# Performance work log

Hardware: AMD Instinct MI355X
Metric: run time of the kernel (lower is better)

Reference implementation:

```python
import jax, jax.numpy as jnp
import numpy as np

LN_EPS = 1e-5

def _layernorm(x, gamma, beta):
    # x: [B, 4, H]; gamma/beta: [4, H]; computed in fp32 as the torch subclass does
    x32 = x.astype(jnp.float32)
    mu = jnp.mean(x32, axis=-1, keepdims=True)
    var = jnp.mean(jnp.square(x32 - mu), axis=-1, keepdims=True)
    y = (x32 - mu) * jax.lax.rsqrt(var + LN_EPS)
    return (y * gamma + beta).astype(x.dtype)

def setup_inputs() -> dict:
    key = jax.random.key(0)
    ks = jax.random.split(key, 6)
    B, I, H = 8192, 512, 1024
    x = jax.random.normal(ks[0], (B, I), dtype=jnp.float32)
    h = jax.random.normal(ks[1], (B, H), dtype=jnp.float32)
    c = jax.random.normal(ks[2], (B, H), dtype=jnp.float32)
    Wi = jax.random.normal(ks[3], (I, 4 * H), dtype=jnp.float32) * (1.0 / np.sqrt(I))
    Wh = jax.random.normal(ks[4], (H, 4 * H), dtype=jnp.float32) * (1.0 / np.sqrt(H))
    bh = jax.random.normal(ks[5], (4 * H,), dtype=jnp.float32) * 0.01
    ln_gamma = jnp.ones((4, H), dtype=jnp.float32)
    ln_beta = jnp.zeros((4, H), dtype=jnp.float32)
    return {"x": x, "h": h, "c": c, "Wi": Wi, "Wh": Wh, "bh": bh,
            "ln_gamma": ln_gamma, "ln_beta": ln_beta}

def reference(x, h, c, Wi, Wh, bh, ln_gamma, ln_beta):
    B = x.shape[0]
    H = h.shape[-1]
    gates = x @ Wi + h @ Wh + bh            # [B, 4H]
    gates = gates.reshape(B, 4, H)           # chunk into i, f, g, o
    gates = _layernorm(gates, ln_gamma, ln_beta)
    i, f, g, o = gates[:, 0], gates[:, 1], gates[:, 2], gates[:, 3]
    c_new = jax.nn.sigmoid(f) * c + jax.nn.sigmoid(i) * jnp.tanh(g)
    h_new = jax.nn.sigmoid(o) * jnp.tanh(c_new)   # layer_norm_c is Identity
    return (h_new, c_new)
```

## Files before the change

kernel.cpp:

```cpp
#include <hip/hip_runtime.h>
#include <stdint.h>

#define BATCH 8192
#define IDIM  512
#define HDIM  1024
#define KDIM  1536
#define NDIM  4096

typedef __bf16 bf16x8 __attribute__((ext_vector_type(8)));
typedef float  f32x4  __attribute__((ext_vector_type(4)));
typedef unsigned short u16x8 __attribute__((ext_vector_type(8)));

__device__ __forceinline__ unsigned short f2bf(float f) {
    union { float f; unsigned u; } v; v.f = f;
    unsigned r = v.u + 0x7fffu + ((v.u >> 16) & 1u);
    return (unsigned short)(r >> 16);
}
__device__ __forceinline__ float bf2f(unsigned short u) {
    union { unsigned u; float f; } v; v.u = ((unsigned)u) << 16;
    return v.f;
}
__device__ __forceinline__ float fexp(float x) {
    return __builtin_amdgcn_exp2f(x * 1.44269504f);
}
__device__ __forceinline__ float sigm(float x) {
    return __builtin_amdgcn_rcpf(1.f + fexp(-x));
}
__device__ __forceinline__ float ftanh(float x) {
    return 1.f - 2.f * __builtin_amdgcn_rcpf(1.f + fexp(2.f * x));
}

__device__ __forceinline__ void load16(void* lds, const void* g) {
    __builtin_amdgcn_global_load_lds(
        (const __attribute__((address_space(1))) unsigned int*)g,
        (__attribute__((address_space(3))) unsigned int*)lds, 16, 0, 0);
}

#define NPACKA (BATCH * KDIM / 4 / 256)
#define NPACKW ((NDIM / 32) * (KDIM / 32))
__global__ __launch_bounds__(256) void pack_ab(const float* __restrict__ x,
                                               const float* __restrict__ h,
                                               const float* __restrict__ Wi,
                                               const float* __restrict__ Wh,
                                               unsigned short* __restrict__ A,
                                               unsigned short* __restrict__ Wt) {
    __shared__ float tile[32][33];
    int blk = blockIdx.x;
    if (blk < NPACKA) {
        int idx = blk * 256 + threadIdx.x;
        int row = idx / (KDIM / 4);
        int g   = idx % (KDIM / 4);
        int col = g * 4;
        float4 v;
        if (col < IDIM) v = ((const float4*)(x + (size_t)row * IDIM))[g];
        else            v = ((const float4*)(h + (size_t)row * HDIM))[(col - IDIM) / 4];
        ushort4 o;
        o.x = f2bf(v.x); o.y = f2bf(v.y); o.z = f2bf(v.z); o.w = f2bf(v.w);
        ((ushort4*)A)[idx] = o;
    } else {
        int b  = blk - NPACKA;
        int n0 = (b & 127) * 32;
        int k0 = (b >> 7) * 32;
        int tx = threadIdx.x & 31, ty = threadIdx.x >> 5;
#pragma unroll
        for (int j = 0; j < 4; j++) {
            int k = k0 + ty + 8 * j;
            float v;
            if (k < IDIM) v = Wi[(size_t)k * NDIM + n0 + tx];
            else          v = Wh[(size_t)(k - IDIM) * NDIM + n0 + tx];
            tile[ty + 8 * j][tx] = v;
        }
        __syncthreads();
#pragma unroll
        for (int j = 0; j < 4; j++)
            Wt[(size_t)(n0 + ty + 8 * j) * KDIM + k0 + tx] = f2bf(tile[tx][ty + 8 * j]);
    }
}

__global__ __launch_bounds__(512, 2) void gemm_bt(const unsigned short* __restrict__ A,
                                                  const unsigned short* __restrict__ Bt,
                                                  unsigned short* __restrict__ C) {
    __shared__ __align__(16) unsigned short smem[65536];

    const int t    = threadIdx.x;
    const int wave = t >> 6;
    const int lane = t & 63;
    const int lrow = lane & 15;
    const int quad = lane >> 4;

    const int bid = blockIdx.x;
    const int xcd = bid & 7;
    const int jj  = bid >> 3;
    const int bm  = (xcd * 4 + (jj & 3)) * 256;
    const int bn  = (jj >> 2) * 256;

    const int wm = (wave & 1) * 128;
    const int wn = (wave >> 1) * 64;

    int srcA[2], srcB[2];
#pragma unroll
    for (int j = 0; j < 2; j++) {
        int q   = t + 512 * j;
        int rp  = q >> 3, s = q & 7;
        int xx  = s ^ (rp & 7);
        int row = 2 * rp + (xx >> 2);
        int kc  = xx & 3;
        srcA[j] = (bm + row) * KDIM + kc * 8;
        srcB[j] = (bn + row) * KDIM + kc * 8;
    }

    int offA[8], offB[4];
#pragma unroll
    for (int mt = 0; mt < 8; mt++) {
        int r = wm + mt * 16 + lrow;
        offA[mt] = (r >> 1) * 64 + (((((r & 1) << 2) | quad) ^ ((r >> 1) & 7)) * 8);
    }
#pragma unroll
    for (int nt = 0; nt < 4; nt++) {
        int r = wn + nt * 16 + lrow;
        offB[nt] = (r >> 1) * 64 + (((((r & 1) << 2) | quad) ^ ((r >> 1) & 7)) * 8);
    }

    f32x4 acc[8][4] = {};

#define STAGE(tt) do {                                              \
    unsigned short* _d = smem + (((tt) & 3) << 14);                 \
    const int _ko = (tt) * 32;                                      \
    load16(_d +          t * 8, A  + (size_t)(srcA[0] + _ko));      \
    load16(_d +  4096 +  t * 8, A  + (size_t)(srcA[1] + _ko));      \
    load16(_d +  8192 +  t * 8, Bt + (size_t)(srcB[0] + _ko));      \
    load16(_d + 12288 +  t * 8, Bt + (size_t)(srcB[1] + _ko));      \
} while (0)

    STAGE(0); STAGE(1); STAGE(2);

    const int NT = KDIM / 32;
    for (int T = 0; T < NT; ++T) {
        if (T < NT - 2)       asm volatile("s_waitcnt vmcnt(8)" ::: "memory");
        else if (T == NT - 2) asm volatile("s_waitcnt vmcnt(4)" ::: "memory");
        else                  asm volatile("s_waitcnt vmcnt(0)" ::: "memory");
        __builtin_amdgcn_s_barrier();
        __builtin_amdgcn_sched_barrier(0);

        const unsigned short* bufA = smem + ((T & 3) << 14);
        const unsigned short* bufB = bufA + 8192;

        bf16x8 a[8], b[4];
        a[0] = *(const bf16x8*)(bufA + offA[0]);
        b[0] = *(const bf16x8*)(bufB + offB[0]);
        b[1] = *(const bf16x8*)(bufB + offB[1]);
        b[2] = *(const bf16x8*)(bufB + offB[2]);
        b[3] = *(const bf16x8*)(bufB + offB[3]);
        if (T + 3 < NT) STAGE(T + 3);

#pragma unroll
        for (int mt = 0; mt < 8; mt++) {
            if (mt < 7) a[mt + 1] = *(const bf16x8*)(bufA + offA[mt + 1]);
#pragma unroll
            for (int nt = 0; nt < 4; nt++)
                acc[mt][nt] = __builtin_amdgcn_mfma_f32_16x16x32_bf16(
                    a[mt], b[nt], acc[mt][nt], 0, 0, 0);
        }
    }
#undef STAGE

#pragma unroll
    for (int mt = 0; mt < 8; mt++)
#pragma unroll
        for (int nt = 0; nt < 4; nt++) {
            int row = bm + wm + mt * 16 + quad * 4;
            int col = bn + wn + nt * 16 + lrow;
#pragma unroll
            for (int r = 0; r < 4; r++)
                C[(size_t)(row + r) * NDIM + col] = f2bf(acc[mt][nt][r]);
        }
}

__global__ __launch_bounds__(256) void lstm_ep(const unsigned short* __restrict__ gates,
                                               const float* __restrict__ bh,
                                               const float* __restrict__ c,
                                               const float* __restrict__ gamma,
                                               const float* __restrict__ beta,
                                               float* __restrict__ out) {
    const int wave = threadIdx.x >> 6;
    const int lane = threadIdx.x & 63;
    const int b    = blockIdx.x * 4 + wave;
    const int col0 = lane * 16;

    const unsigned short* gr = gates + (size_t)b * NDIM;
    float v[4][16];
    float s[4], sq[4];
#pragma unroll
    for (int g = 0; g < 4; g++) {
        const unsigned short* gp = gr + g * HDIM + col0;
        u16x8 ga = *(const u16x8*)gp;
        u16x8 gb = *(const u16x8*)(gp + 8);
        float bb[16];
#pragma unroll
        for (int q = 0; q < 4; q++)
            *(float4*)(bb + 4 * q) = ((const float4*)(bh + g * HDIM + col0))[q];
        float ls = 0.f, lq = 0.f;
#pragma unroll
        for (int j = 0; j < 16; j++) {
            float tv = bf2f(j < 8 ? ga[j] : gb[j - 8]) + bb[j];
            v[g][j] = tv; ls += tv; lq += tv * tv;
        }
        s[g] = ls; sq[g] = lq;
    }
#pragma unroll
    for (int off = 32; off; off >>= 1) {
#pragma unroll
        for (int g = 0; g < 4; g++) {
            s[g]  += __shfl_xor(s[g], off);
            sq[g] += __shfl_xor(sq[g], off);
        }
    }
#pragma unroll
    for (int g = 0; g < 4; g++) {
        const float mu  = s[g] * (1.f / HDIM);
        const float var = sq[g] * (1.f / HDIM) - mu * mu;
        const float rs  = rsqrtf(var + 1e-5f);
        float gm[16], bt[16];
#pragma unroll
        for (int q = 0; q < 4; q++) {
            *(float4*)(gm + 4 * q) = ((const float4*)(gamma + g * HDIM + col0))[q];
            *(float4*)(bt + 4 * q) = ((const float4*)(beta  + g * HDIM + col0))[q];
        }
#pragma unroll
        for (int j = 0; j < 16; j++) {
            float y = (v[g][j] - mu) * rs * gm[j] + bt[j];
            v[g][j] = (g == 2) ? ftanh(y) : sigm(y);
        }
    }
    const size_t base = (size_t)b * HDIM + col0;
#pragma unroll
    for (int q = 0; q < 4; q++) {
        float4 ci = *(const float4*)(c + base + 4 * q);
        float4 cn, hn;
#pragma unroll
        for (int e = 0; e < 4; e++) {
            int j = 4 * q + e;
            float cnv = v[1][j] * ((float*)&ci)[e] + v[0][j] * v[2][j];
            ((float*)&cn)[e] = cnv;
            ((float*)&hn)[e] = v[3][j] * ftanh(cnv);
        }
        *(float4*)(out + base + 4 * q) = hn;
        *(float4*)(out + (size_t)BATCH * HDIM + base + 4 * q) = cn;
    }
}

extern "C" void kernel_launch(void* const* d_in, const int* in_sizes, int n_in,
                              void* d_out, int out_size, void* d_ws, size_t ws_size,
                              hipStream_t stream) {
    const float* x     = (const float*)d_in[0];
    const float* h     = (const float*)d_in[1];
    const float* c     = (const float*)d_in[2];
    const float* Wi    = (const float*)d_in[3];
    const float* Wh    = (const float*)d_in[4];
    const float* bh    = (const float*)d_in[5];
    const float* gamma = (const float*)d_in[6];
    const float* beta  = (const float*)d_in[7];
    float* out = (float*)d_out;

    unsigned short* A  = (unsigned short*)d_ws;
    unsigned short* Wt = (unsigned short*)((char*)d_ws + (size_t)BATCH * KDIM * 2);
    unsigned short* gates = (unsigned short*)((char*)d_ws + (size_t)BATCH * KDIM * 2
                                                          + (size_t)NDIM * KDIM * 2);

    pack_ab<<<NPACKA + NPACKW, 256, 0, stream>>>(x, h, Wi, Wh, A, Wt);
    gemm_bt<<<dim3((BATCH / 256) * (NDIM / 256)), 512, 0, stream>>>(A, Wt, gates);
    lstm_ep<<<BATCH / 4, 256, 0, stream>>>(gates, bh, c, gamma, beta, out);
}
```

Measured before the change: 298.3 us.

## Pack operands into MFMA fragment layout and load directly from global memory

Packs A and the transposed weights into a fragment-contiguous layout so each MFMA operand fragment is one coalesced 16-byte-per-lane load. The GEMM drops the LDS staging, barriers and swizzle and instead double-buffers fragments in registers straight from global memory. This removes LDS traffic and synchronisation but loses intra-block operand sharing, so waves re-read the same tiles from L2, and latency hiding relies on a single prefetch stage.

```diff
diff --git a/kernel.cpp b/kernel.cpp
--- a/kernel.cpp
+++ b/kernel.cpp
@@ -6,6 +6,7 @@
 #define HDIM  1024
 #define KDIM  1536
 #define NDIM  4096
+#define NKT   (KDIM / 32)
 
 typedef __bf16 bf16x8 __attribute__((ext_vector_type(8)));
 typedef float  f32x4  __attribute__((ext_vector_type(4)));
@@ -30,10 +31,9 @@
     return 1.f - 2.f * __builtin_amdgcn_rcpf(1.f + fexp(2.f * x));
 }
 
-__device__ __forceinline__ void load16(void* lds, const void* g) {
-    __builtin_amdgcn_global_load_lds(
-        (const __attribute__((address_space(1))) unsigned int*)g,
-        (__attribute__((address_space(3))) unsigned int*)lds, 16, 0, 0);
+__device__ __forceinline__ size_t frag_addr(int row, int k) {
+    return ((size_t)((row >> 4) * NKT + (k >> 5)) << 9)
+         + (((row & 15) + 16 * ((k >> 3) & 3)) << 3) + (k & 7);
 }
 
 #define NPACKA (BATCH * KDIM / 4 / 256)
@@ -56,7 +56,7 @@
         else            v = ((const float4*)(h + (size_t)row * HDIM))[(col - IDIM) / 4];
         ushort4 o;
         o.x = f2bf(v.x); o.y = f2bf(v.y); o.z = f2bf(v.z); o.w = f2bf(v.w);
-        ((ushort4*)A)[idx] = o;
+        *(ushort4*)(A + frag_addr(row, col)) = o;
     } else {
         int b  = blk - NPACKA;
         int n0 = (b & 127) * 32;
@@ -72,21 +72,23 @@
         }
         __syncthreads();
 #pragma unroll
-        for (int j = 0; j < 4; j++)
-            Wt[(size_t)(n0 + ty + 8 * j) * KDIM + k0 + tx] = f2bf(tile[tx][ty + 8 * j]);
+        for (int j = 0; j < 4; j++) {
+            int n = n0 + ty + 8 * j;
+            int k = k0 + tx;
+            Wt[frag_addr(n, k)] = f2bf(tile[tx][ty + 8 * j]);
+        }
     }
 }
 
 __global__ __launch_bounds__(512, 2) void gemm_bt(const unsigned short* __restrict__ A,
                                                   const unsigned short* __restrict__ Bt,
                                                   unsigned short* __restrict__ C) {
-    __shared__ __align__(16) unsigned short smem[65536];
-
     const int t    = threadIdx.x;
     const int wave = t >> 6;
     const int lane = t & 63;
     const int lrow = lane & 15;
     const int quad = lane >> 4;
+    const int l8   = lane * 8;
 
     const int bid = blockIdx.x;
     const int xcd = bid & 7;
@@ -96,73 +98,37 @@
 
     const int wm = (wave & 1) * 128;
     const int wn = (wave >> 1) * 64;
-
-    int srcA[2], srcB[2];
-#pragma unroll
-    for (int j = 0; j < 2; j++) {
-        int q   = t + 512 * j;
-        int rp  = q >> 3, s = q & 7;
-        int xx  = s ^ (rp & 7);
-        int row = 2 * rp + (xx >> 2);
-        int kc  = xx & 3;
-        srcA[j] = (bm + row) * KDIM + kc * 8;
-        srcB[j] = (bn + row) * KDIM + kc * 8;
-    }
-
-    int offA[8], offB[4];
-#pragma unroll
-    for (int mt = 0; mt < 8; mt++) {
-        int r = wm + mt * 16 + lrow;
-        offA[mt] = (r >> 1) * 64 + (((((r & 1) << 2) | quad) ^ ((r >> 1) & 7)) * 8);
-    }
-#pragma unroll
-    for (int nt = 0; nt < 4; nt++) {
-        int r = wn + nt * 16 + lrow;
-        offB[nt] = (r >> 1) * 64 + (((((r & 1) << 2) | quad) ^ ((r >> 1) & 7)) * 8);
-    }
+    const int m16w = (bm + wm) >> 4;
+    const int n16w = (bn + wn) >> 4;
 
     f32x4 acc[8][4] = {};
 
-#define STAGE(tt) do {                                              \
-    unsigned short* _d = smem + (((tt) & 3) << 14);                 \
-    const int _ko = (tt) * 32;                                      \
-    load16(_d +          t * 8, A  + (size_t)(srcA[0] + _ko));      \
-    load16(_d +  4096 +  t * 8, A  + (size_t)(srcA[1] + _ko));      \
-    load16(_d +  8192 +  t * 8, Bt + (size_t)(srcB[0] + _ko));      \
-    load16(_d + 12288 +  t * 8, Bt + (size_t)(srcB[1] + _ko));      \
-} while (0)
-
-    STAGE(0); STAGE(1); STAGE(2);
-
-    const int NT = KDIM / 32;
-    for (int T = 0; T < NT; ++T) {
-        if (T < NT - 2)       asm volatile("s_waitcnt vmcnt(8)" ::: "memory");
-        else if (T == NT - 2) asm volatile("s_waitcnt vmcnt(4)" ::: "memory");
-        else                  asm volatile("s_waitcnt vmcnt(0)" ::: "memory");
-        __builtin_amdgcn_s_barrier();
-        __builtin_amdgcn_sched_barrier(0);
-
-        const unsigned short* bufA = smem + ((T & 3) << 14);
-        const unsigned short* bufB = bufA + 8192;
-
-        bf16x8 a[8], b[4];
-        a[0] = *(const bf16x8*)(bufA + offA[0]);
-        b[0] = *(const bf16x8*)(bufB + offB[0]);
-        b[1] = *(const bf16x8*)(bufB + offB[1]);
-        b[2] = *(const bf16x8*)(bufB + offB[2]);
-        b[3] = *(const bf16x8*)(bufB + offB[3]);
-        if (T + 3 < NT) STAGE(T + 3);
-
-#pragma unroll
-        for (int mt = 0; mt < 8; mt++) {
-            if (mt < 7) a[mt + 1] = *(const bf16x8*)(bufA + offA[mt + 1]);
-#pragma unroll
-            for (int nt = 0; nt < 4; nt++)
-                acc[mt][nt] = __builtin_amdgcn_mfma_f32_16x16x32_bf16(
-                    a[mt], b[nt], acc[mt][nt], 0, 0, 0);
-        }
-    }
-#undef STAGE
+#define LOAD_SET(aa, bb, ktv) {                                                     \
+    _Pragma("unroll")                                                               \
+    for (int mt = 0; mt < 8; mt++)                                                  \
+        aa[mt] = *(const bf16x8*)(A + ((size_t)((m16w + mt) * NKT + (ktv)) << 9) + l8); \
+    _Pragma("unroll")                                                               \
+    for (int nt = 0; nt < 4; nt++)                                                  \
+        bb[nt] = *(const bf16x8*)(Bt + ((size_t)((n16w + nt) * NKT + (ktv)) << 9) + l8); }
+
+#define MFMA_SET(aa, bb) {                                                          \
+    _Pragma("unroll")                                                               \
+    for (int mt = 0; mt < 8; mt++)                                                  \
+        _Pragma("unroll")                                                           \
+        for (int nt = 0; nt < 4; nt++)                                              \
+            acc[mt][nt] = __builtin_amdgcn_mfma_f32_16x16x32_bf16(                  \
+                aa[mt], bb[nt], acc[mt][nt], 0, 0, 0); }
+
+    bf16x8 a0[8], b0[4], a1[8], b1[4];
+    LOAD_SET(a0, b0, 0);
+    for (int kt = 0; kt < NKT; kt += 2) {
+        LOAD_SET(a1, b1, kt + 1);
+        MFMA_SET(a0, b0);
+        if (kt + 2 < NKT) LOAD_SET(a0, b0, kt + 2);
+        MFMA_SET(a1, b1);
+    }
+#undef LOAD_SET
+#undef MFMA_SET
 
 #pragma unroll
     for (int mt = 0; mt < 8; mt++)
```

After: 324.7 us. 1.09x slower.
